# Optimization experiments

Measured on AMD Instinct MI355X. Metric: run time of the kernel, lower is better.

## Reference

```python
import jax, jax.numpy as jnp
import numpy as np

N, M, D = 8192, 8192, 512
TINY = jnp.finfo(jnp.float32).tiny


def setup_inputs() -> dict:
    key = jax.random.key(0)
    k1, k2 = jax.random.split(key)
    x = jax.random.normal(k1, (N, D), dtype=jnp.float32)
    x2 = jax.random.normal(k2, (M, D), dtype=jnp.float32)
    # flax self.param with ones initializer (pre-softplus raw params)
    amplitude_raw = jnp.ones((1,), dtype=jnp.float32)
    length_scale_raw = jnp.ones((D,), dtype=jnp.float32)
    return {"x": x, "x2": x2, "amplitude_raw": amplitude_raw,
            "length_scale_raw": length_scale_raw}


def reference(x, x2, amplitude_raw, length_scale_raw):
    # Parameter transforms exactly as in RBFKernelProvider.apply
    amplitude = jax.nn.softplus(amplitude_raw) + TINY          # (1,)
    length_scale = jax.nn.softplus(length_scale_raw) + TINY    # (D,)

    # rbf_kernel_fun: exp(-0.5 * sum(((x - x2)/l)^2)) * amp^2
    # GEMM rewrite of the squared scaled distance (avoids (N,M,D) intermediate):
    # ||xs_i - ys_j||^2 = ||xs_i||^2 + ||ys_j||^2 - 2 xs_i . ys_j
    xs = x / length_scale                                       # (N, D)
    ys = x2 / length_scale                                      # (M, D)
    x_sq = jnp.sum(xs * xs, axis=-1)                            # (N,)
    y_sq = jnp.sum(ys * ys, axis=-1)                            # (M,)
    cross = jnp.einsum('nd,md->nm', xs, ys)                     # (N, M) GEMM
    sq_dists = jnp.maximum(x_sq[:, None] + y_sq[None, :] - 2.0 * cross, 0.0)
    kernel_matrix = jnp.exp(-0.5 * sq_dists)                    # (N, M)
    return (amplitude ** 2) * kernel_matrix
```

## Files before the change

### kernel.cpp

```cpp
#include <hip/hip_runtime.h>

#define AS1 __attribute__((address_space(1)))
#define AS3 __attribute__((address_space(3)))

typedef __attribute__((ext_vector_type(4))) float f32x4;
typedef __attribute__((ext_vector_type(8))) int   i32x8;

static constexpr int Nn = 8192;
static constexpr int Mm = 8192;
static constexpr int Dd = 512;
static constexpr float TINY = 1.17549435082228751e-38f;

__device__ __forceinline__ float softplus_f(float x) {
    return fmaxf(x, 0.0f) + log1pf(expf(-fabsf(x)));
}

__device__ __forceinline__ void g2l16(const void* g, void* l) {
    __builtin_amdgcn_global_load_lds((const AS1 unsigned int*)g,
                                     (AS3 unsigned int*)l, 16, 0, 0);
}

__global__ __launch_bounds__(256) void scale_rows(
        const float* __restrict__ x, const float* __restrict__ x2,
        const float* __restrict__ ls_raw,
        unsigned char* __restrict__ xs, unsigned char* __restrict__ ys,
        float* __restrict__ x_sq, float* __restrict__ y_sq) {
    int wave = threadIdx.x >> 6, lane = threadIdx.x & 63;
    int row = blockIdx.x * 4 + wave;

    const float* src; unsigned char* dst; float* nrm; int r;
    if (row < Nn) {
        src = x  + (size_t)row * Dd; dst = xs + (size_t)row * 512;
        nrm = x_sq + row; r = row;
    } else {
        int m = row - Nn;
        src = x2 + (size_t)m * Dd;   dst = ys + (size_t)m * 512;
        nrm = y_sq + m; r = m;
    }

    float4 v0 = ((const float4*)src)[lane * 2];
    float4 v1 = ((const float4*)src)[lane * 2 + 1];
    float4 L0 = ((const float4*)ls_raw)[lane * 2];
    float4 L1 = ((const float4*)ls_raw)[lane * 2 + 1];

    float il[8] = {
        1.0f / (softplus_f(L0.x) + TINY), 1.0f / (softplus_f(L0.y) + TINY),
        1.0f / (softplus_f(L0.z) + TINY), 1.0f / (softplus_f(L0.w) + TINY),
        1.0f / (softplus_f(L1.x) + TINY), 1.0f / (softplus_f(L1.y) + TINY),
        1.0f / (softplus_f(L1.z) + TINY), 1.0f / (softplus_f(L1.w) + TINY) };
    float s[8] = { v0.x*il[0], v0.y*il[1], v0.z*il[2], v0.w*il[3],
                   v1.x*il[4], v1.y*il[5], v1.z*il[6], v1.w*il[7] };
    float sum = 0.0f;
#pragma unroll
    for (int i = 0; i < 8; ++i) sum += s[i] * s[i];

    int p0 = __builtin_amdgcn_cvt_pk_fp8_f32(s[0], s[1], 0, false);
    p0     = __builtin_amdgcn_cvt_pk_fp8_f32(s[2], s[3], p0, true);
    int p1 = __builtin_amdgcn_cvt_pk_fp8_f32(s[4], s[5], 0, false);
    p1     = __builtin_amdgcn_cvt_pk_fp8_f32(s[6], s[7], p1, true);

    int j    = lane >> 1;
    int phys = (j & ~7) | ((j & 7) ^ (r & 7));
    *(int2*)(dst + phys * 16 + (lane & 1) * 8) = make_int2(p0, p1);

#pragma unroll
    for (int off = 32; off > 0; off >>= 1) sum += __shfl_down(sum, off, 64);
    if (lane == 0) *nrm = sum;
}

__global__ __launch_bounds__(256) void gemm_rbf(
        const unsigned char* __restrict__ xs,
        const unsigned char* __restrict__ ys,
        const float* __restrict__ x_sq, const float* __restrict__ y_sq,
        const float* __restrict__ amp_raw, float* __restrict__ out) {

    __shared__ unsigned char sA[128 * 128];
    __shared__ unsigned char sB[128 * 128];

    const int tid  = threadIdx.x;
    const int wave = tid >> 6, lane = tid & 63;
    const int wy = wave >> 1, wx = wave & 1;
    const int lane15 = lane & 15, quad = lane >> 4;
    const int srow = lane >> 3, schunk = lane & 7;

    const size_t rowBase = (size_t)blockIdx.y * 128;
    const size_t colBase = (size_t)blockIdx.x * 128;

    f32x4 acc[4][4] = {};

    for (int kt = 0; kt < 4; ++kt) {
        __syncthreads();
        const size_t kOff = (size_t)kt * 128;
#pragma unroll
        for (int t = 0; t < 4; ++t) {
            int issue = wave * 4 + t;
            int rit = issue * 8 + srow;
            const unsigned char* ga =
                xs + (rowBase + rit) * 512 + kOff + schunk * 16;
            g2l16(ga, sA + issue * 1024);
            const unsigned char* gb =
                ys + (colBase + rit) * 512 + kOff + schunk * 16;
            g2l16(gb, sB + issue * 1024);
        }
        __syncthreads();

        i32x8 xF[4];
#pragma unroll
        for (int ty = 0; ty < 4; ++ty) {
            int rr = wy * 64 + ty * 16 + lane15;
            int x7 = rr & 7;
            int p0 = (quad * 2 + 0) ^ x7, p1 = (quad * 2 + 1) ^ x7;
            int4 lo = *(const int4*)(sA + rr * 128 + p0 * 16);
            int4 hi = *(const int4*)(sA + rr * 128 + p1 * 16);
            i32x8 f; f[0]=lo.x; f[1]=lo.y; f[2]=lo.z; f[3]=lo.w;
                     f[4]=hi.x; f[5]=hi.y; f[6]=hi.z; f[7]=hi.w;
            xF[ty] = f;
        }
#pragma unroll
        for (int tx = 0; tx < 4; ++tx) {
            int rr = wx * 64 + tx * 16 + lane15;
            int x7 = rr & 7;
            int p0 = (quad * 2 + 0) ^ x7, p1 = (quad * 2 + 1) ^ x7;
            int4 lo = *(const int4*)(sB + rr * 128 + p0 * 16);
            int4 hi = *(const int4*)(sB + rr * 128 + p1 * 16);
            i32x8 yF; yF[0]=lo.x; yF[1]=lo.y; yF[2]=lo.z; yF[3]=lo.w;
                      yF[4]=hi.x; yF[5]=hi.y; yF[6]=hi.z; yF[7]=hi.w;
#pragma unroll
            for (int ty = 0; ty < 4; ++ty)
                acc[ty][tx] = __builtin_amdgcn_mfma_scale_f32_16x16x128_f8f6f4(
                    yF, xF[ty], acc[ty][tx],
                    0 , 0 ,
                    0, 0x7F7F7F7F,
                    0, 0x7F7F7F7F);
        }
    }

    float a = softplus_f(amp_raw[0]) + TINY;
    const float amp2 = a * a;
#pragma unroll
    for (int ty = 0; ty < 4; ++ty) {
        const size_t n = rowBase + wy * 64 + ty * 16 + lane15;
        const float xq = x_sq[n];
        float* orow = out + n * (size_t)Mm;
#pragma unroll
        for (int tx = 0; tx < 4; ++tx) {
            const size_t m0 = colBase + wx * 64 + tx * 16 + quad * 4;
            const float4 yq = *(const float4*)(y_sq + m0);
            float4 r;
            r.x = amp2 * __expf(-0.5f * fmaxf(xq + yq.x - 2.0f * acc[ty][tx][0], 0.0f));
            r.y = amp2 * __expf(-0.5f * fmaxf(xq + yq.y - 2.0f * acc[ty][tx][1], 0.0f));
            r.z = amp2 * __expf(-0.5f * fmaxf(xq + yq.z - 2.0f * acc[ty][tx][2], 0.0f));
            r.w = amp2 * __expf(-0.5f * fmaxf(xq + yq.w - 2.0f * acc[ty][tx][3], 0.0f));
            *(float4*)(orow + m0) = r;
        }
    }
}

__global__ __launch_bounds__(256) void rbf_fallback(
        const float* __restrict__ x, const float* __restrict__ x2,
        const float* __restrict__ amp_raw, const float* __restrict__ ls_raw,
        float* __restrict__ out) {
    __shared__ float il[Dd];
    __shared__ float sX[16 * Dd];
    __shared__ float sY[16 * Dd];
    int tid = threadIdx.x;
    for (int i = tid; i < Dd; i += 256)
        il[i] = 1.0f / (softplus_f(ls_raw[i]) + TINY);
    __syncthreads();
    int bR = blockIdx.y * 16, bC = blockIdx.x * 16;
    for (int i = tid; i < 16 * Dd; i += 256) {
        int r = i >> 9, c = i & (Dd - 1);
        sX[i] = x [(size_t)(bR + r) * Dd + c] * il[c];
        sY[i] = x2[(size_t)(bC + r) * Dd + c] * il[c];
    }
    __syncthreads();
    float a = softplus_f(amp_raw[0]) + TINY;
    float amp2 = a * a;
    int r = tid >> 4, c = tid & 15;
    float sq = 0.0f;
    for (int d = 0; d < Dd; ++d) {
        float df = sX[r * Dd + d] - sY[c * Dd + d];
        sq += df * df;
    }
    out[(size_t)(bR + r) * Mm + (bC + c)] = amp2 * __expf(-0.5f * sq);
}

extern "C" void kernel_launch(void* const* d_in, const int* in_sizes, int n_in,
                              void* d_out, int out_size, void* d_ws, size_t ws_size,
                              hipStream_t stream) {
    const float* x       = (const float*)d_in[0];
    const float* x2      = (const float*)d_in[1];
    const float* amp_raw = (const float*)d_in[2];
    const float* ls_raw  = (const float*)d_in[3];
    float* out = (float*)d_out;

    const size_t OFF_XSQ = 0;
    const size_t OFF_YSQ = OFF_XSQ + 8192 * 4;
    const size_t OFF_XS  = OFF_YSQ + 8192 * 4;
    const size_t OFF_YS  = OFF_XS + (size_t)Nn * Dd;
    const size_t NEED    = OFF_YS + (size_t)Mm * Dd;

    if (ws_size < NEED) {
        dim3 g(Mm / 16, Nn / 16);
        rbf_fallback<<<g, 256, 0, stream>>>(x, x2, amp_raw, ls_raw, out);
        return;
    }

    char* ws = (char*)d_ws;
    float* x_sq = (float*)(ws + OFF_XSQ);
    float* y_sq = (float*)(ws + OFF_YSQ);
    unsigned char* xs = (unsigned char*)(ws + OFF_XS);
    unsigned char* ys = (unsigned char*)(ws + OFF_YS);

    scale_rows<<<(Nn + Mm) / 4, 256, 0, stream>>>(x, x2, ls_raw, xs, ys, x_sq, y_sq);
    dim3 g(Mm / 128, Nn / 128);
    gemm_rbf<<<g, 256, 0, stream>>>(xs, ys, x_sq, y_sq, amp_raw, out);
}
```

Measured before the change: 342.1 us.

## Load FP8 MFMA fragments straight from global memory, skipping LDS staging

The GEMM kernel drops the shared-memory tiles, the global_load_lds copies and the barriers. Each wave now reads its MFMA operand fragments directly from global memory (L2/L1), and the loop is fully unrolled. The scale_rows kernel writes the fp8 data in a permuted order so every lane's fragment sits at contiguous 16-byte offsets. This removes synchronisation and LDS traffic, but the two waves sharing a row or column tile now fetch the same data separately, which raises cache traffic and loses reuse across waves.

```diff
diff --git a/kernel.cpp b/kernel.cpp
--- a/kernel.cpp
+++ b/kernel.cpp
@@ -1,7 +1,4 @@
 #include <hip/hip_runtime.h>
-
-#define AS1 __attribute__((address_space(1)))
-#define AS3 __attribute__((address_space(3)))
 
 typedef __attribute__((ext_vector_type(4))) float f32x4;
 typedef __attribute__((ext_vector_type(8))) int   i32x8;
@@ -15,11 +12,6 @@
     return fmaxf(x, 0.0f) + log1pf(expf(-fabsf(x)));
 }
 
-__device__ __forceinline__ void g2l16(const void* g, void* l) {
-    __builtin_amdgcn_global_load_lds((const AS1 unsigned int*)g,
-                                     (AS3 unsigned int*)l, 16, 0, 0);
-}
-
 __global__ __launch_bounds__(256) void scale_rows(
         const float* __restrict__ x, const float* __restrict__ x2,
         const float* __restrict__ ls_raw,
@@ -28,14 +20,14 @@
     int wave = threadIdx.x >> 6, lane = threadIdx.x & 63;
     int row = blockIdx.x * 4 + wave;
 
-    const float* src; unsigned char* dst; float* nrm; int r;
+    const float* src; unsigned char* dst; float* nrm;
     if (row < Nn) {
         src = x  + (size_t)row * Dd; dst = xs + (size_t)row * 512;
-        nrm = x_sq + row; r = row;
+        nrm = x_sq + row;
     } else {
         int m = row - Nn;
         src = x2 + (size_t)m * Dd;   dst = ys + (size_t)m * 512;
-        nrm = y_sq + m; r = m;
+        nrm = y_sq + m;
     }
 
     float4 v0 = ((const float4*)src)[lane * 2];
@@ -59,9 +51,9 @@
     int p1 = __builtin_amdgcn_cvt_pk_fp8_f32(s[4], s[5], 0, false);
     p1     = __builtin_amdgcn_cvt_pk_fp8_f32(s[6], s[7], p1, true);
 
-    int j    = lane >> 1;
-    int phys = (j & ~7) | ((j & 7) ^ (r & 7));
-    *(int2*)(dst + phys * 16 + (lane & 1) * 8) = make_int2(p0, p1);
+    int dest = (lane >> 4) * 128 + ((lane & 3) >> 1) * 64
+             + (((lane & 15) >> 2) * 16) + 8 * (lane & 1);
+    *(int2*)(dst + dest) = make_int2(p0, p1);
 
 #pragma unroll
     for (int off = 32; off > 0; off >>= 1) sum += __shfl_down(sum, off, 64);
@@ -74,55 +66,37 @@
         const float* __restrict__ x_sq, const float* __restrict__ y_sq,
         const float* __restrict__ amp_raw, float* __restrict__ out) {
 
-    __shared__ unsigned char sA[128 * 128];
-    __shared__ unsigned char sB[128 * 128];
-
     const int tid  = threadIdx.x;
     const int wave = tid >> 6, lane = tid & 63;
     const int wy = wave >> 1, wx = wave & 1;
     const int lane15 = lane & 15, quad = lane >> 4;
-    const int srow = lane >> 3, schunk = lane & 7;
 
     const size_t rowBase = (size_t)blockIdx.y * 128;
     const size_t colBase = (size_t)blockIdx.x * 128;
 
+    const unsigned char* xbase = xs + (rowBase + wy * 64 + lane15) * 512 + quad * 16;
+    const unsigned char* ybase = ys + (colBase + wx * 64 + lane15) * 512 + quad * 16;
+
     f32x4 acc[4][4] = {};
 
+#pragma unroll
     for (int kt = 0; kt < 4; ++kt) {
-        __syncthreads();
         const size_t kOff = (size_t)kt * 128;
-#pragma unroll
-        for (int t = 0; t < 4; ++t) {
-            int issue = wave * 4 + t;
-            int rit = issue * 8 + srow;
-            const unsigned char* ga =
-                xs + (rowBase + rit) * 512 + kOff + schunk * 16;
-            g2l16(ga, sA + issue * 1024);
-            const unsigned char* gb =
-                ys + (colBase + rit) * 512 + kOff + schunk * 16;
-            g2l16(gb, sB + issue * 1024);
-        }
-        __syncthreads();
-
         i32x8 xF[4];
 #pragma unroll
         for (int ty = 0; ty < 4; ++ty) {
-            int rr = wy * 64 + ty * 16 + lane15;
-            int x7 = rr & 7;
-            int p0 = (quad * 2 + 0) ^ x7, p1 = (quad * 2 + 1) ^ x7;
-            int4 lo = *(const int4*)(sA + rr * 128 + p0 * 16);
-            int4 hi = *(const int4*)(sA + rr * 128 + p1 * 16);
+            const unsigned char* p = xbase + (size_t)ty * 16 * 512 + kOff;
+            int4 lo = *(const int4*)p;
+            int4 hi = *(const int4*)(p + 64);
             i32x8 f; f[0]=lo.x; f[1]=lo.y; f[2]=lo.z; f[3]=lo.w;
                      f[4]=hi.x; f[5]=hi.y; f[6]=hi.z; f[7]=hi.w;
             xF[ty] = f;
         }
 #pragma unroll
         for (int tx = 0; tx < 4; ++tx) {
-            int rr = wx * 64 + tx * 16 + lane15;
-            int x7 = rr & 7;
-            int p0 = (quad * 2 + 0) ^ x7, p1 = (quad * 2 + 1) ^ x7;
-            int4 lo = *(const int4*)(sB + rr * 128 + p0 * 16);
-            int4 hi = *(const int4*)(sB + rr * 128 + p1 * 16);
+            const unsigned char* p = ybase + (size_t)tx * 16 * 512 + kOff;
+            int4 lo = *(const int4*)p;
+            int4 hi = *(const int4*)(p + 64);
             i32x8 yF; yF[0]=lo.x; yF[1]=lo.y; yF[2]=lo.z; yF[3]=lo.w;
                       yF[4]=hi.x; yF[5]=hi.y; yF[6]=hi.z; yF[7]=hi.w;
 #pragma unroll
```

Measured after the change: 420.8 us. 23.0% more time.

## Double-buffer LDS staging and shrink GEMM tile to 128x64

Applied to the files above, without the earlier changes.

Splits the LDS A/B tiles into two buffers so the async global-to-LDS loads for the next K step are issued while MFMAs run on the current one. This drops one barrier per iteration. It also halves the N tile from 128 to 64 columns, doubling the grid and reducing per-wave accumulators, which helps more workgroups fit and overlap their epilogue writes. The cost is less reuse of the A tile per block and more total global traffic. Correctness relies on the async LDS loads completing before the single barrier.

```diff
diff --git a/kernel.cpp b/kernel.cpp
--- a/kernel.cpp
+++ b/kernel.cpp
@@ -74,8 +74,8 @@
         const float* __restrict__ x_sq, const float* __restrict__ y_sq,
         const float* __restrict__ amp_raw, float* __restrict__ out) {
 
-    __shared__ unsigned char sA[128 * 128];
-    __shared__ unsigned char sB[128 * 128];
+    __shared__ unsigned char sA[2][128 * 128];
+    __shared__ unsigned char sB[2][64 * 128];
 
     const int tid  = threadIdx.x;
     const int wave = tid >> 6, lane = tid & 63;
@@ -84,25 +84,37 @@
     const int srow = lane >> 3, schunk = lane & 7;
 
     const size_t rowBase = (size_t)blockIdx.y * 128;
-    const size_t colBase = (size_t)blockIdx.x * 128;
-
-    f32x4 acc[4][4] = {};
-
+    const size_t colBase = (size_t)blockIdx.x * 64;
+
+    f32x4 acc[4][2] = {};
+
+    auto stage = [&](int kt, int b) {
+        const size_t kOff = (size_t)kt * 128;
+#pragma unroll
+        for (int t = 0; t < 4; ++t) {
+            int idx = wave * 4 + t;
+            int rit = idx * 8 + srow;
+            const unsigned char* ga =
+                xs + (rowBase + rit) * 512 + kOff + schunk * 16;
+            g2l16(ga, &sA[b][idx * 1024]);
+        }
+#pragma unroll
+        for (int u = 0; u < 2; ++u) {
+            int idx = wave * 2 + u;
+            int rit = idx * 8 + srow;
+            const unsigned char* gb =
+                ys + (colBase + rit) * 512 + kOff + schunk * 16;
+            g2l16(gb, &sB[b][idx * 1024]);
+        }
+    };
+
+    stage(0, 0);
+
+#pragma unroll
     for (int kt = 0; kt < 4; ++kt) {
         __syncthreads();
-        const size_t kOff = (size_t)kt * 128;
-#pragma unroll
-        for (int t = 0; t < 4; ++t) {
-            int issue = wave * 4 + t;
-            int rit = issue * 8 + srow;
-            const unsigned char* ga =
-                xs + (rowBase + rit) * 512 + kOff + schunk * 16;
-            g2l16(ga, sA + issue * 1024);
-            const unsigned char* gb =
-                ys + (colBase + rit) * 512 + kOff + schunk * 16;
-            g2l16(gb, sB + issue * 1024);
-        }
-        __syncthreads();
+        if (kt < 3) stage(kt + 1, (kt + 1) & 1);
+        const int b = kt & 1;
 
         i32x8 xF[4];
 #pragma unroll
@@ -110,19 +122,19 @@
             int rr = wy * 64 + ty * 16 + lane15;
             int x7 = rr & 7;
             int p0 = (quad * 2 + 0) ^ x7, p1 = (quad * 2 + 1) ^ x7;
-            int4 lo = *(const int4*)(sA + rr * 128 + p0 * 16);
-            int4 hi = *(const int4*)(sA + rr * 128 + p1 * 16);
+            int4 lo = *(const int4*)(&sA[b][rr * 128 + p0 * 16]);
+            int4 hi = *(const int4*)(&sA[b][rr * 128 + p1 * 16]);
             i32x8 f; f[0]=lo.x; f[1]=lo.y; f[2]=lo.z; f[3]=lo.w;
                      f[4]=hi.x; f[5]=hi.y; f[6]=hi.z; f[7]=hi.w;
             xF[ty] = f;
         }
 #pragma unroll
-        for (int tx = 0; tx < 4; ++tx) {
-            int rr = wx * 64 + tx * 16 + lane15;
+        for (int tx = 0; tx < 2; ++tx) {
+            int rr = wx * 32 + tx * 16 + lane15;
             int x7 = rr & 7;
             int p0 = (quad * 2 + 0) ^ x7, p1 = (quad * 2 + 1) ^ x7;
-            int4 lo = *(const int4*)(sB + rr * 128 + p0 * 16);
-            int4 hi = *(const int4*)(sB + rr * 128 + p1 * 16);
+            int4 lo = *(const int4*)(&sB[b][rr * 128 + p0 * 16]);
+            int4 hi = *(const int4*)(&sB[b][rr * 128 + p1 * 16]);
             i32x8 yF; yF[0]=lo.x; yF[1]=lo.y; yF[2]=lo.z; yF[3]=lo.w;
                       yF[4]=hi.x; yF[5]=hi.y; yF[6]=hi.z; yF[7]=hi.w;
 #pragma unroll
@@ -143,8 +155,8 @@
         const float xq = x_sq[n];
         float* orow = out + n * (size_t)Mm;
 #pragma unroll
-        for (int tx = 0; tx < 4; ++tx) {
-            const size_t m0 = colBase + wx * 64 + tx * 16 + quad * 4;
+        for (int tx = 0; tx < 2; ++tx) {
+            const size_t m0 = colBase + wx * 32 + tx * 16 + quad * 4;
             const float4 yq = *(const float4*)(y_sq + m0);
             float4 r;
             r.x = amp2 * __expf(-0.5f * fmaxf(xq + yq.x - 2.0f * acc[ty][tx][0], 0.0f));
@@ -213,6 +225,6 @@
     unsigned char* ys = (unsigned char*)(ws + OFF_YS);
 
     scale_rows<<<(Nn + Mm) / 4, 256, 0, stream>>>(x, x2, ls_raw, xs, ys, x_sq, y_sq);
-    dim3 g(Mm / 128, Nn / 128);
+    dim3 g(Mm / 64, Nn / 128);
     gemm_rbf<<<g, 256, 0, stream>>>(xs, ys, x_sq, y_sq, amp_raw, out);
 }
```

Result: no change. 339.8 us (-0.7%).
